# Performance work log

Hardware: AMD Instinct MI355X
Metric: run time of the kernel (lower is better)

Reference implementation:

```python
import jax, jax.numpy as jnp
import numpy as np

B, N, D, H, HID = 8, 512, 512, 8, 2048


def setup_inputs() -> dict:
    key = jax.random.key(0)
    ks = jax.random.split(key, 8)
    s = 0.02
    p = lambda i, shape: jax.random.normal(ks[i], shape, jnp.float32) * s
    return dict(
        x=jax.random.normal(ks[0], (B, N, D), jnp.float32),
        Wq=p(1, (D, D)), bq=jnp.zeros((D,), jnp.float32),
        Wk=p(2, (D, D)), bk=jnp.zeros((D,), jnp.float32),
        Wv=p(3, (D, D)), bv=jnp.zeros((D,), jnp.float32),
        Wsig=p(4, (H, D)), bsig=jnp.zeros((H,), jnp.float32),
        ln1_g=jnp.ones((D,), jnp.float32), ln1_b=jnp.zeros((D,), jnp.float32),
        W1=p(5, (HID, D)), b1=jnp.zeros((HID,), jnp.float32),
        W2=p(6, (D, HID)), b2=jnp.zeros((D,), jnp.float32),
        ln2_g=jnp.ones((D,), jnp.float32), ln2_b=jnp.zeros((D,), jnp.float32),
    )


def _ln(z, g, b, eps=1e-5):
    m = jnp.mean(z, axis=-1, keepdims=True)
    v = jnp.var(z, axis=-1, keepdims=True)
    return (z - m) * jax.lax.rsqrt(v + eps) * g + b


def reference(x, Wq, bq, Wk, bk, Wv, bv, Wsig, bsig,
              ln1_g, ln1_b, W1, b1, W2, b2, ln2_g, ln2_b):
    Bb, Nn, Dd = x.shape
    Hh = bsig.shape[0]
    dh = Dd // Hh
    # --- AnomalyAttention: series attention S, Gaussian prior P, Z = S @ V ---
    Q = (x @ Wq.T + bq).reshape(Bb, Nn, Hh, dh)
    K = (x @ Wk.T + bk).reshape(Bb, Nn, Hh, dh)
    V = (x @ Wv.T + bv).reshape(Bb, Nn, Hh, dh)
    scores = jnp.einsum('bnhd,bmhd->bhnm', Q, K) / jnp.sqrt(jnp.float32(dh))
    S = jax.nn.softmax(scores, axis=-1)                       # [B,H,N,N]
    # learned positive scale sigma per (batch, position, head)
    sigma = jax.nn.softplus(x @ Wsig.T + bsig) + 1e-5         # [B,N,H]
    idx = jnp.arange(Nn, dtype=jnp.float32)
    dist2 = (idx[:, None] - idx[None, :]) ** 2                # [N,N]
    sig = jnp.transpose(sigma, (0, 2, 1))[..., None]          # [B,H,N,1]
    gauss = jnp.exp(-dist2 / (2.0 * sig * sig)) / (jnp.sqrt(2.0 * jnp.pi) * sig)
    P = gauss / jnp.sum(gauss, axis=-1, keepdims=True)        # row-normalized prior
    Zh = jnp.einsum('bhnm,bmhd->bnhd', S, V).reshape(Bb, Nn, Dd)
    # --- residual + LayerNorm + MLP(relu) + residual + LayerNorm ---
    Z = _ln(Zh + x, ln1_g, ln1_b)
    hidden = jax.nn.relu(Z @ W1.T + b1)
    x_hat = hidden @ W2.T + b2
    x_hat = _ln(x_hat + Z, ln2_g, ln2_b)
    return (x_hat, P, S)
```

## Files before the change

### kernel.cpp

```cpp
#include <hip/hip_runtime.h>
#include <cstdint>

typedef short s16x8 __attribute__((ext_vector_type(8)));
typedef float f32x4 __attribute__((ext_vector_type(4)));
using u16 = unsigned short;


__device__ __forceinline__ u16 f2bf(float f) {
    union { float f; uint32_t u; } v; v.f = f;
    uint32_t u = v.u;
    return (u16)((u + 0x7FFFu + ((u >> 16) & 1u)) >> 16);
}
__device__ __forceinline__ float bf2f(u16 u) {
    return __uint_as_float(((uint32_t)u) << 16);
}

__device__ __forceinline__ void gload_lds16(const void* g, void* l) {
    __builtin_amdgcn_global_load_lds(
        (const __attribute__((address_space(1))) unsigned int*)g,
        (__attribute__((address_space(3))) unsigned int*)l, 16, 0, 0);
}

__global__ __launch_bounds__(256) void k_convert_sigma(
    const float* __restrict__ x, const float* __restrict__ wq,
    const float* __restrict__ wk, const float* __restrict__ wv,
    const float* __restrict__ w1, const float* __restrict__ w2,
    const float* __restrict__ bq, const float* __restrict__ bk,
    const float* __restrict__ bv,
    const float* __restrict__ Wsig, const float* __restrict__ bsig,
    u16* __restrict__ xb, u16* __restrict__ wqb, u16* __restrict__ wkb,
    u16* __restrict__ wvb, u16* __restrict__ w1b, u16* __restrict__ w2b,
    float* __restrict__ biascat, float* __restrict__ sigT)
{
    int bk_ = blockIdx.x;
    int tid = threadIdx.x;
    if (bk_ >= 4866) {
        int row  = (int)(((bk_ - 4866) * 256 + tid) >> 6);
        int lane = tid & 63;
        const float4* xr = (const float4*)(x + (long)row * 512);
        float4 xa = xr[lane * 2], xc = xr[lane * 2 + 1];
        float xs[8] = {xa.x, xa.y, xa.z, xa.w, xc.x, xc.y, xc.z, xc.w};
        float ph[8];
#pragma unroll
        for (int h = 0; h < 8; ++h) {
            const float4* wr = (const float4*)(Wsig + h * 512);
            float4 wa = wr[lane * 2], wc = wr[lane * 2 + 1];
            ph[h] = xs[0]*wa.x + xs[1]*wa.y + xs[2]*wa.z + xs[3]*wa.w
                  + xs[4]*wc.x + xs[5]*wc.y + xs[6]*wc.z + xs[7]*wc.w;
        }
#pragma unroll
        for (int h = 0; h < 8; ++h)
#pragma unroll
            for (int m = 1; m < 64; m <<= 1)
                ph[h] += __shfl_xor(ph[h], m, 64);
        if (lane < 8) {
            float z  = ph[lane] + bsig[lane];
            float sp = fmaxf(z, 0.f) + log1pf(__expf(-fabsf(z)));
            int b = row >> 9, n = row & 511;
            sigT[(((long)b * 8 + lane) << 9) + n] = sp + 1e-5f;
        }
        return;
    }
    long g = (long)bk_ * 256 + tid;
    if (g >= 1245184) {
        long id = g - 1245184;
        if (id < 384) {
            const float* src = id < 128 ? bq : id < 256 ? bk : bv;
            ((float4*)biascat)[id] = ((const float4*)src)[id & 127];
        }
        return;
    }
    const float* src; u16* dst; long off;
    if      (g <  524288) { src = x;  dst = xb;  off = g; }
    else if (g <  589824) { src = wq; dst = wqb; off = g -  524288; }
    else if (g <  655360) { src = wk; dst = wkb; off = g -  589824; }
    else if (g <  720896) { src = wv; dst = wvb; off = g -  655360; }
    else if (g <  983040) { src = w1; dst = w1b; off = g -  720896; }
    else                  { src = w2; dst = w2b; off = g -  983040; }
    float4 v = ((const float4*)src)[off];
    ushort4 o;
    o.x = f2bf(v.x); o.y = f2bf(v.y); o.z = f2bf(v.z); o.w = f2bf(v.w);
    ((ushort4*)dst)[off] = o;
}

template<int BM, int BN, int EPI>
__global__ __launch_bounds__(512) void k_gemm_nt(
    const u16* __restrict__ A, const u16* __restrict__ B,
    const float* __restrict__ bias, void* __restrict__ C,
    int lda, int ldb, int K)
{
    constexpr int BK = 64;
    __shared__ __align__(16) u16 As[2][BM * BK];
    __shared__ __align__(16) u16 Bs[2][BN * BK];

    const u16* Ag = A + (long)blockIdx.x * BM * lda;
    const u16* Bg = B + (long)blockIdx.y * BN * ldb;

    int tid  = threadIdx.x;
    int wave = tid >> 6, lane = tid & 63;
    int wm = wave >> 2, wn = wave & 3;
    constexpr int WTM = BM / 2, WTN = BN / 4;
    constexpr int FM = WTM / 16, FN = WTN / 16;
    int r16 = lane & 15, g4 = lane >> 4;

    f32x4 acc[FM][FN];
#pragma unroll
    for (int i = 0; i < FM; ++i)
#pragma unroll
        for (int j = 0; j < FN; ++j) acc[i][j] = (f32x4){0.f, 0.f, 0.f, 0.f};

    constexpr int nA = BM * BK / (512 * 8);
    constexpr int nB = BN * BK / (512 * 8);

    auto stage = [&](int buf, int k0) {
#pragma unroll
        for (int c = 0; c < nA; ++c) {
            int e = c * 512 + tid;
            int r = e >> 3, s = e & 7;
            gload_lds16(Ag + (long)r * lda + k0 + ((s ^ (r & 7)) * 8),
                        &As[buf][e * 8]);
        }
#pragma unroll
        for (int c = 0; c < nB; ++c) {
            int e = c * 512 + tid;
            int r = e >> 3, s = e & 7;
            gload_lds16(Bg + (long)r * ldb + k0 + ((s ^ (r & 7)) * 8),
                        &Bs[buf][e * 8]);
        }
    };

    stage(0, 0);
    __syncthreads();
    int cur = 0;
    const int NT = K / BK;
    for (int t = 0; t < NT; ++t) {
        if (t + 1 < NT) stage(cur ^ 1, (t + 1) * BK);
#pragma unroll
        for (int kk = 0; kk < 2; ++kk) {
            s16x8 af[FM], bfr[FN];
#pragma unroll
            for (int fm = 0; fm < FM; ++fm) {
                int row = wm * WTM + fm * 16 + r16;
                int slot = (kk * 4 + g4) ^ (row & 7);
                af[fm] = *(const s16x8*)&As[cur][row * 64 + slot * 8];
            }
#pragma unroll
            for (int fn = 0; fn < FN; ++fn) {
                int row = wn * WTN + fn * 16 + r16;
                int slot = (kk * 4 + g4) ^ (row & 7);
                bfr[fn] = *(const s16x8*)&Bs[cur][row * 64 + slot * 8];
            }
#pragma unroll
            for (int fm = 0; fm < FM; ++fm)
#pragma unroll
                for (int fn = 0; fn < FN; ++fn)
                    acc[fm][fn] = __builtin_amdgcn_mfma_f32_16x16x32_bf16(af[fm], bfr[fn], acc[fm][fn], 0, 0, 0);
        }
        __syncthreads();
        cur ^= 1;
    }

    int i0 = blockIdx.x * BM + wm * WTM;
    int j0 = blockIdx.y * BN + wn * WTN;
#pragma unroll
    for (int fm = 0; fm < FM; ++fm)
#pragma unroll
        for (int fn = 0; fn < FN; ++fn)
#pragma unroll
            for (int j = 0; j < 4; ++j) {
                int gi = i0 + fm * 16 + (g4 << 2) + j;
                int gj = j0 + fn * 16 + r16;
                float v = acc[fm][fn][j];
                if constexpr (EPI == 3) {
                    v = fmaxf(v + bias[gj], 0.f);
                    ((u16*)C)[(long)gi * 2048 + gj] = f2bf(v);
                } else if constexpr (EPI == 4) {
                    ((float*)C)[(long)gi * 512 + gj] = v + bias[gj];
                } else {
                    v += bias[gj];
                    int mat = gj >> 9, cj = gj & 511;
                    int h = cj >> 6, d = cj & 63, b = gi >> 9, n = gi & 511;
                    u16* base = (u16*)C;
                    if (mat == 0)
                        base[(((long)(b * 8 + h) * 512 + n) << 6) + d] = f2bf(v);
                    else if (mat == 1)
                        (base + 2097152)[(((long)(b * 8 + h) * 512 + n) << 6) + d] = f2bf(v);
                    else
                        (base + 4194304)[(((long)(b * 8 + h) * 64 + d) << 9) + n] = f2bf(v);
                }
            }
}

__global__ __launch_bounds__(256) void k_attn_prior(
    const u16* __restrict__ Qb, const u16* __restrict__ Kb,
    const u16* __restrict__ Vt, const float* __restrict__ sigT,
    float* __restrict__ S, float* __restrict__ Zh, float* __restrict__ P)
{
    __shared__ __align__(16) u16 Sb[4][16][264];
    __shared__ float cmbM[2][2][16];
    __shared__ float cmbS[2][2][16];
    __shared__ float zc[2][16][66];

    int gid = blockIdx.x;
    int tid = threadIdx.x;
    int wave = tid >> 6, lane = tid & 63;

    if (gid >= 1024) {
        int row = (gid - 1024) * 4 + wave;
        int n = row & 511;
        float s = sigT[row];
        float a = -1.0f / (2.0f * s * s);
        float e[8]; float sum = 0.f;
#pragma unroll
        for (int j = 0; j < 8; ++j) {
            float d = (float)(n - (lane * 8 + j));
            e[j] = __expf(a * d * d);
            sum += e[j];
        }
#pragma unroll
        for (int m = 1; m < 64; m <<= 1) sum += __shfl_xor(sum, m, 64);
        float r = 1.0f / sum;
        f32x4* dst = (f32x4*)(P + (long)row * 512 + lane * 8);
        dst[0] = (f32x4){e[0]*r, e[1]*r, e[2]*r, e[3]*r};
        dst[1] = (f32x4){e[4]*r, e[5]*r, e[6]*r, e[7]*r};
        return;
    }

    int bh = gid & 63;
    int rb = gid >> 6;
    int rg = wave >> 1, ch = wave & 1;
    int r16 = lane & 15, g4 = lane >> 4, hi8 = g4 * 8;

    int row0 = rb * 32 + rg * 16;
    const u16* Qg = Qb + ((long)bh * 512 + row0) * 64;
    const u16* Kg = Kb + ((long)bh * 512 + ch * 256) * 64;
    const u16* Vg = Vt + (long)bh * 64 * 512;

    s16x8 qa[2];
    qa[0] = *(const s16x8*)(Qg + r16 * 64 + hi8);
    qa[1] = *(const s16x8*)(Qg + r16 * 64 + 32 + hi8);

    f32x4 acc[16];
#pragma unroll
    for (int t = 0; t < 16; ++t) acc[t] = (f32x4){0.f, 0.f, 0.f, 0.f};

    __builtin_amdgcn_s_setprio(1);
#pragma unroll
    for (int kk = 0; kk < 2; ++kk)
#pragma unroll
        for (int t = 0; t < 16; ++t) {
            s16x8 b = *(const s16x8*)(Kg + (long)(t * 16 + r16) * 64 + kk * 32 + hi8);
            acc[t] = __builtin_amdgcn_mfma_f32_16x16x32_bf16(qa[kk], b, acc[t], 0, 0, 0);
        }
    __builtin_amdgcn_s_setprio(0);

    float mx[4] = {-1e30f, -1e30f, -1e30f, -1e30f};
#pragma unroll
    for (int t = 0; t < 16; ++t)
#pragma unroll
        for (int j = 0; j < 4; ++j) mx[j] = fmaxf(mx[j], acc[t][j]);
#pragma unroll
    for (int j = 0; j < 4; ++j)
#pragma unroll
        for (int m = 1; m < 16; m <<= 1) mx[j] = fmaxf(mx[j], __shfl_xor(mx[j], m, 64));

    float sm[4] = {0.f, 0.f, 0.f, 0.f};
#pragma unroll
    for (int t = 0; t < 16; ++t)
#pragma unroll
        for (int j = 0; j < 4; ++j) {
            float p = __expf(0.125f * (acc[t][j] - mx[j]));
            acc[t][j] = p;
            sm[j] += p;
        }
#pragma unroll
    for (int j = 0; j < 4; ++j)
#pragma unroll
        for (int m = 1; m < 16; m <<= 1) sm[j] += __shfl_xor(sm[j], m, 64);

    if (r16 == 0) {
#pragma unroll
        for (int j = 0; j < 4; ++j) {
            cmbM[rg][ch][g4 * 4 + j] = mx[j];
            cmbS[rg][ch][g4 * 4 + j] = sm[j];
        }
    }
    __syncthreads();

    float scale[4];
#pragma unroll
    for (int j = 0; j < 4; ++j) {
        float mo = cmbM[rg][ch ^ 1][g4 * 4 + j];
        float so = cmbS[rg][ch ^ 1][g4 * 4 + j];
        float M  = fmaxf(mx[j], mo);
        float tot = sm[j] * __expf(mx[j] - M) + so * __expf(mo - M);
        scale[j] = __expf(mx[j] - M) / tot;
    }
#pragma unroll
    for (int t = 0; t < 16; ++t)
#pragma unroll
        for (int j = 0; j < 4; ++j) acc[t][j] *= scale[j];

#pragma unroll
    for (int t = 0; t < 16; ++t)
#pragma unroll
        for (int j = 0; j < 4; ++j)
            Sb[wave][g4 * 4 + j][t * 16 + r16] = f2bf(acc[t][j]);

    long sbase = ((long)bh * 512 + row0) * 512 + ch * 256;
#pragma unroll
    for (int r = 0; r < 16; ++r) {
        ushort4 u = *(const ushort4*)&Sb[wave][r][lane * 4];
        *(f32x4*)&S[sbase + (long)r * 512 + lane * 4] =
            (f32x4){bf2f(u.x), bf2f(u.y), bf2f(u.z), bf2f(u.w)};
    }

    f32x4 zacc[4];
#pragma unroll
    for (int fn = 0; fn < 4; ++fn) zacc[fn] = (f32x4){0.f, 0.f, 0.f, 0.f};

    __builtin_amdgcn_s_setprio(1);
#pragma unroll
    for (int kb = 0; kb < 8; ++kb) {
        s16x8 pa = *(const s16x8*)&Sb[wave][r16][kb * 32 + hi8];
#pragma unroll
        for (int fn = 0; fn < 4; ++fn) {
            s16x8 vb = *(const s16x8*)(Vg + (long)(fn * 16 + r16) * 512 + ch * 256 + kb * 32 + hi8);
            zacc[fn] = __builtin_amdgcn_mfma_f32_16x16x32_bf16(pa, vb, zacc[fn], 0, 0, 0);
        }
    }
    __builtin_amdgcn_s_setprio(0);

    if (ch == 1) {
#pragma unroll
        for (int fn = 0; fn < 4; ++fn)
#pragma unroll
            for (int j = 0; j < 4; ++j)
                zc[rg][g4 * 4 + j][fn * 16 + r16] = zacc[fn][j];
    }
    __syncthreads();
    if (ch == 0) {
        long zb = ((long)(bh >> 3) * 512 + row0) * 512 + (bh & 7) * 64;
#pragma unroll
        for (int fn = 0; fn < 4; ++fn)
#pragma unroll
            for (int j = 0; j < 4; ++j)
                Zh[zb + (long)(g4 * 4 + j) * 512 + fn * 16 + r16] =
                    zacc[fn][j] + zc[rg][g4 * 4 + j][fn * 16 + r16];
    }
}

template<bool WBF>
__global__ __launch_bounds__(256) void k_ln(
    const float* __restrict__ a, const float* __restrict__ b,
    const float* __restrict__ g, const float* __restrict__ bt,
    float* __restrict__ y, u16* __restrict__ yb)
{
    int row  = (int)((blockIdx.x * 256 + threadIdx.x) >> 6);
    int lane = threadIdx.x & 63;
    const float4* ar = (const float4*)(a + (long)row * 512);
    const float4* br = (const float4*)(b + (long)row * 512);
    float4 a0 = ar[lane * 2], a1 = ar[lane * 2 + 1];
    float4 b0 = br[lane * 2], b1 = br[lane * 2 + 1];
    float v[8] = {a0.x + b0.x, a0.y + b0.y, a0.z + b0.z, a0.w + b0.w,
                  a1.x + b1.x, a1.y + b1.y, a1.z + b1.z, a1.w + b1.w};
    float s = 0.f, q = 0.f;
#pragma unroll
    for (int j = 0; j < 8; ++j) { s += v[j]; q += v[j] * v[j]; }
#pragma unroll
    for (int m = 1; m < 64; m <<= 1) {
        s += __shfl_xor(s, m, 64);
        q += __shfl_xor(q, m, 64);
    }
    float mean = s * (1.f / 512.f);
    float var  = q * (1.f / 512.f) - mean * mean;
    float rstd = rsqrtf(var + 1e-5f);
    const float4* gr = (const float4*)(g + lane * 8);
    const float4* tr = (const float4*)(bt + lane * 8);
    float4 g0 = gr[0], g1 = gr[1], t0 = tr[0], t1 = tr[1];
    float gg[8] = {g0.x, g0.y, g0.z, g0.w, g1.x, g1.y, g1.z, g1.w};
    float tt[8] = {t0.x, t0.y, t0.z, t0.w, t1.x, t1.y, t1.z, t1.w};
    float o[8];
#pragma unroll
    for (int j = 0; j < 8; ++j) o[j] = (v[j] - mean) * rstd * gg[j] + tt[j];
    float4* yr = (float4*)(y + (long)row * 512 + lane * 8);
    yr[0] = make_float4(o[0], o[1], o[2], o[3]);
    yr[1] = make_float4(o[4], o[5], o[6], o[7]);
    if constexpr (WBF) {
        s16x8 ob;
#pragma unroll
        for (int j = 0; j < 8; ++j) ob[j] = (short)f2bf(o[j]);
        *(s16x8*)(yb + (long)row * 512 + lane * 8) = ob;
    }
}

extern "C" void kernel_launch(void* const* d_in, const int* in_sizes, int n_in,
                              void* d_out, int out_size, void* d_ws, size_t ws_size,
                              hipStream_t stream)
{
    const float* x    = (const float*)d_in[0];
    const float* Wq   = (const float*)d_in[1];
    const float* bq   = (const float*)d_in[2];
    const float* Wk   = (const float*)d_in[3];
    const float* bk   = (const float*)d_in[4];
    const float* Wv   = (const float*)d_in[5];
    const float* bv   = (const float*)d_in[6];
    const float* Wsig = (const float*)d_in[7];
    const float* bsig = (const float*)d_in[8];
    const float* g1   = (const float*)d_in[9];
    const float* be1  = (const float*)d_in[10];
    const float* W1   = (const float*)d_in[11];
    const float* b1   = (const float*)d_in[12];
    const float* W2   = (const float*)d_in[13];
    const float* b2   = (const float*)d_in[14];
    const float* g2   = (const float*)d_in[15];
    const float* be2  = (const float*)d_in[16];

    float* out_xhat = (float*)d_out;
    float* out_P    = out_xhat + 2097152;
    float* out_S    = out_P + 16777216;

    char* ws = (char*)d_ws;
    u16*   xb   = (u16*)(ws + 0);
    u16*   Qb   = (u16*)(ws + 4194304);
    u16*   hid  = (u16*)(ws + 0);
    u16*   Wqb  = (u16*)(ws + 16777216);
    u16*   W1b  = (u16*)(ws + 18350080);
    u16*   W2b  = (u16*)(ws + 20447232);
    float* sigT = (float*)(ws + 22544384);
    float* Zh   = (float*)(ws + 22675456);
    float* bcat = (float*)(ws + 22675456);
    float* x2   = (float*)(ws + 22675456);
    float* Z    = (float*)(ws + 31064064);
    u16*   Zb   = (u16*)(ws + 39452672);

    u16* Wkb = Wqb + 262144;
    u16* Wvb = Wqb + 524288;

    k_convert_sigma<<<5890, 256, 0, stream>>>(x, Wq, Wk, Wv, W1, W2, bq, bk, bv,
                                              Wsig, bsig,
                                              xb, Wqb, Wkb, Wvb, W1b, W2b,
                                              bcat, sigT);

    k_gemm_nt<128,128,5><<<dim3(32,12,1),512,0,stream>>>(
        xb, Wqb, bcat, Qb, 512, 512, 512);

    k_attn_prior<<<9216, 256, 0, stream>>>(Qb, Qb + 2097152, Qb + 4194304,
                                           sigT, out_S, Zh, out_P);

    k_ln<true><<<1024,256,0,stream>>>(Zh, x, g1, be1, Z, Zb);

    k_gemm_nt<128,128,3><<<dim3(32,16,1),512,0,stream>>>(Zb, W1b, b1, hid, 512, 512, 512);

    k_gemm_nt<64,128,4><<<dim3(64,4,1),512,0,stream>>>(hid, W2b, b2, x2, 2048, 2048, 2048);

    k_ln<false><<<1024,256,0,stream>>>(x2, Z, g2, be2, out_xhat, nullptr);
}
```

Before: 135.0 us.

## Move Gaussian prior work into MLP1 GEMM launch and reorder attention stores

```diff
diff --git a/kernel.cpp b/kernel.cpp
--- a/kernel.cpp
+++ b/kernel.cpp
@@ -84,17 +84,15 @@
 }
 
 template<int BM, int BN, int EPI>
-__global__ __launch_bounds__(512) void k_gemm_nt(
+__device__ __forceinline__ void gemm_body(
     const u16* __restrict__ A, const u16* __restrict__ B,
     const float* __restrict__ bias, void* __restrict__ C,
-    int lda, int ldb, int K)
+    int lda, int ldb, int K, int bx, int by,
+    u16* __restrict__ As, u16* __restrict__ Bs)
 {
     constexpr int BK = 64;
-    __shared__ __align__(16) u16 As[2][BM * BK];
-    __shared__ __align__(16) u16 Bs[2][BN * BK];
-
-    const u16* Ag = A + (long)blockIdx.x * BM * lda;
-    const u16* Bg = B + (long)blockIdx.y * BN * ldb;
+    const u16* Ag = A + (long)bx * BM * lda;
+    const u16* Bg = B + (long)by * BN * ldb;
 
     int tid  = threadIdx.x;
     int wave = tid >> 6, lane = tid & 63;
@@ -118,14 +116,14 @@
             int e = c * 512 + tid;
             int r = e >> 3, s = e & 7;
             gload_lds16(Ag + (long)r * lda + k0 + ((s ^ (r & 7)) * 8),
-                        &As[buf][e * 8]);
+                        &As[buf * BM * BK + e * 8]);
         }
 #pragma unroll
         for (int c = 0; c < nB; ++c) {
             int e = c * 512 + tid;
             int r = e >> 3, s = e & 7;
             gload_lds16(Bg + (long)r * ldb + k0 + ((s ^ (r & 7)) * 8),
-                        &Bs[buf][e * 8]);
+                        &Bs[buf * BN * BK + e * 8]);
         }
     };
 
@@ -142,13 +140,13 @@
             for (int fm = 0; fm < FM; ++fm) {
                 int row = wm * WTM + fm * 16 + r16;
                 int slot = (kk * 4 + g4) ^ (row & 7);
-                af[fm] = *(const s16x8*)&As[cur][row * 64 + slot * 8];
+                af[fm] = *(const s16x8*)&As[cur * BM * BK + row * 64 + slot * 8];
             }
 #pragma unroll
             for (int fn = 0; fn < FN; ++fn) {
                 int row = wn * WTN + fn * 16 + r16;
                 int slot = (kk * 4 + g4) ^ (row & 7);
-                bfr[fn] = *(const s16x8*)&Bs[cur][row * 64 + slot * 8];
+                bfr[fn] = *(const s16x8*)&Bs[cur * BN * BK + row * 64 + slot * 8];
             }
 #pragma unroll
             for (int fm = 0; fm < FM; ++fm)
@@ -160,8 +158,8 @@
         cur ^= 1;
     }
 
-    int i0 = blockIdx.x * BM + wm * WTM;
-    int j0 = blockIdx.y * BN + wn * WTN;
+    int i0 = bx * BM + wm * WTM;
+    int j0 = by * BN + wn * WTN;
 #pragma unroll
     for (int fm = 0; fm < FM; ++fm)
 #pragma unroll
@@ -191,10 +189,58 @@
             }
 }
 
-__global__ __launch_bounds__(256) void k_attn_prior(
+template<int BM, int BN, int EPI>
+__global__ __launch_bounds__(512) void k_gemm_nt(
+    const u16* __restrict__ A, const u16* __restrict__ B,
+    const float* __restrict__ bias, void* __restrict__ C,
+    int lda, int ldb, int K)
+{
+    __shared__ __align__(16) u16 As[2 * BM * 64];
+    __shared__ __align__(16) u16 Bs[2 * BN * 64];
+    gemm_body<BM, BN, EPI>(A, B, bias, C, lda, ldb, K,
+                           blockIdx.x, blockIdx.y, As, Bs);
+}
+
+__global__ __launch_bounds__(512) void k_mlp1_prior(
+    const u16* __restrict__ Zb, const u16* __restrict__ W1b,
+    const float* __restrict__ b1, u16* __restrict__ hid,
+    const float* __restrict__ sigT, float* __restrict__ P)
+{
+    __shared__ __align__(16) u16 As[2 * 128 * 64];
+    __shared__ __align__(16) u16 Bs[2 * 128 * 64];
+
+    int gid = blockIdx.x;
+    if (gid % 9 == 0) {
+        int gi = gid / 9;
+        gemm_body<128, 128, 3>(Zb, W1b, b1, hid, 512, 512, 512,
+                               gi & 31, gi >> 5, As, Bs);
+        return;
+    }
+    int pid  = gid - gid / 9 - 1;
+    int wave = threadIdx.x >> 6, lane = threadIdx.x & 63;
+    int row  = pid * 8 + wave;
+    int n = row & 511;
+    float s = sigT[row];
+    float a = -1.0f / (2.0f * s * s);
+    float e[8]; float sum = 0.f;
+#pragma unroll
+    for (int j = 0; j < 8; ++j) {
+        float d = (float)(n - (lane * 8 + j));
+        e[j] = __expf(a * d * d);
+        sum += e[j];
+    }
+#pragma unroll
+    for (int m = 1; m < 64; m <<= 1) sum += __shfl_xor(sum, m, 64);
+    float r = 1.0f / sum;
+    f32x4* dst = (f32x4*)(P + (long)row * 512 + lane * 8);
+    dst[0] = (f32x4){e[0]*r, e[1]*r, e[2]*r, e[3]*r};
+    dst[1] = (f32x4){e[4]*r, e[5]*r, e[6]*r, e[7]*r};
+}
+
+__global__ __launch_bounds__(256) void k_attn(
     const u16* __restrict__ Qb, const u16* __restrict__ Kb,
-    const u16* __restrict__ Vt, const float* __restrict__ sigT,
-    float* __restrict__ S, float* __restrict__ Zh, float* __restrict__ P)
+    const u16* __restrict__ Vt,
+    float* __restrict__ S, float* __restrict__ Zh)
 {
     __shared__ __align__(16) u16 Sb[4][16][264];
     __shared__ float cmbM[2][2][16];
@@ -202,32 +248,10 @@
     __shared__ float zc[2][16][66];
 
     int gid = blockIdx.x;
+    int bh = gid & 63;
+    int rb = gid >> 6;
     int tid = threadIdx.x;
     int wave = tid >> 6, lane = tid & 63;
-
-    if (gid >= 1024) {
-        int row = (gid - 1024) * 4 + wave;
-        int n = row & 511;
-        float s = sigT[row];
-        float a = -1.0f / (2.0f * s * s);
-        float e[8]; float sum = 0.f;
-#pragma unroll
-        for (int j = 0; j < 8; ++j) {
-            float d = (float)(n - (lane * 8 + j));
-            e[j] = __expf(a * d * d);
-            sum += e[j];
-        }
-#pragma unroll
-        for (int m = 1; m < 64; m <<= 1) sum += __shfl_xor(sum, m, 64);
-        float r = 1.0f / sum;
-        f32x4* dst = (f32x4*)(P + (long)row * 512 + lane * 8);
-        dst[0] = (f32x4){e[0]*r, e[1]*r, e[2]*r, e[3]*r};
-        dst[1] = (f32x4){e[4]*r, e[5]*r, e[6]*r, e[7]*r};
-        return;
-    }
-
-    int bh = gid & 63;
-    int rb = gid >> 6;
     int rg = wave >> 1, ch = wave & 1;
     int r16 = lane & 15, g4 = lane >> 4, hi8 = g4 * 8;
 
@@ -307,6 +331,22 @@
         for (int j = 0; j < 4; ++j)
             Sb[wave][g4 * 4 + j][t * 16 + r16] = f2bf(acc[t][j]);
 
+    f32x4 zacc[4];
+#pragma unroll
+    for (int fn = 0; fn < 4; ++fn) zacc[fn] = (f32x4){0.f, 0.f, 0.f, 0.f};
+
+    __builtin_amdgcn_s_setprio(1);
+#pragma unroll
+    for (int kb = 0; kb < 8; ++kb) {
+        s16x8 pa = *(const s16x8*)&Sb[wave][r16][kb * 32 + hi8];
+#pragma unroll
+        for (int fn = 0; fn < 4; ++fn) {
+            s16x8 vb = *(const s16x8*)(Vg + (long)(fn * 16 + r16) * 512 + ch * 256 + kb * 32 + hi8);
+            zacc[fn] = __builtin_amdgcn_mfma_f32_16x16x32_bf16(pa, vb, zacc[fn], 0, 0, 0);
+        }
+    }
+    __builtin_amdgcn_s_setprio(0);
+
     long sbase = ((long)bh * 512 + row0) * 512 + ch * 256;
 #pragma unroll
     for (int r = 0; r < 16; ++r) {
@@ -314,22 +354,6 @@
         *(f32x4*)&S[sbase + (long)r * 512 + lane * 4] =
             (f32x4){bf2f(u.x), bf2f(u.y), bf2f(u.z), bf2f(u.w)};
     }
-
-    f32x4 zacc[4];
-#pragma unroll
-    for (int fn = 0; fn < 4; ++fn) zacc[fn] = (f32x4){0.f, 0.f, 0.f, 0.f};
-
-    __builtin_amdgcn_s_setprio(1);
-#pragma unroll
-    for (int kb = 0; kb < 8; ++kb) {
-        s16x8 pa = *(const s16x8*)&Sb[wave][r16][kb * 32 + hi8];
-#pragma unroll
-        for (int fn = 0; fn < 4; ++fn) {
-            s16x8 vb = *(const s16x8*)(Vg + (long)(fn * 16 + r16) * 512 + ch * 256 + kb * 32 + hi8);
-            zacc[fn] = __builtin_amdgcn_mfma_f32_16x16x32_bf16(pa, vb, zacc[fn], 0, 0, 0);
-        }
-    }
-    __builtin_amdgcn_s_setprio(0);
 
     if (ch == 1) {
 #pragma unroll
@@ -445,12 +469,12 @@
     k_gemm_nt<128,128,5><<<dim3(32,12,1),512,0,stream>>>(
         xb, Wqb, bcat, Qb, 512, 512, 512);
 
-    k_attn_prior<<<9216, 256, 0, stream>>>(Qb, Qb + 2097152, Qb + 4194304,
-                                           sigT, out_S, Zh, out_P);
+    k_attn<<<1024, 256, 0, stream>>>(Qb, Qb + 2097152, Qb + 4194304,
+                                     out_S, Zh);
 
     k_ln<true><<<1024,256,0,stream>>>(Zh, x, g1, be1, Z, Zb);
 
-    k_gemm_nt<128,128,3><<<dim3(32,16,1),512,0,stream>>>(Zb, W1b, b1, hid, 512, 512, 512);
+    k_mlp1_prior<<<4608, 512, 0, stream>>>(Zb, W1b, b1, hid, sigT, out_P);
 
     k_gemm_nt<64,128,4><<<dim3(64,4,1),512,0,stream>>>(hid, W2b, b2, x2, 2048, 2048, 2048);
 
```

Result: slower. 141.0 us (+4.4%).
